# Kernel tuning notes

Measured on AMD Instinct MI355X. Metric: run time of the kernel, lower is better.

The kernel has to match this reference:

```python
import jax, jax.numpy as jnp
import numpy as np

N = 20000   # nodes
E = 400000  # edges per hop
IN_C = 256
HID = 128
HEADS = 2
OUT_C = 256
RELU_SLOPE = 0.2  # GATConv LeakyReLU negative slope
EPS = 1e-16


def _segment_mean(vals, idx, num_segments):
    s = jax.ops.segment_sum(vals, idx, num_segments=num_segments)
    cnt = jax.ops.segment_sum(jnp.ones((vals.shape[0], 1), vals.dtype), idx,
                              num_segments=num_segments)
    return s / (cnt + EPS)


def _gat(x, src, dst, Wg, a_src, a_dst, bg):
    # x: [N, IN_C] -> h: [N, HEADS, HID]
    h = (x @ Wg).reshape(N, HEADS, HID)
    alpha_s = jnp.sum(h * a_src, axis=-1)  # [N, HEADS]
    alpha_d = jnp.sum(h * a_dst, axis=-1)  # [N, HEADS]
    logits = jax.nn.leaky_relu(alpha_s[src] + alpha_d[dst], RELU_SLOPE)  # [E, HEADS]
    # softmax over incoming edges per destination node
    m = jax.ops.segment_max(logits, dst, num_segments=N)  # [N, HEADS]
    m = jnp.where(jnp.isfinite(m), m, 0.0)
    ex = jnp.exp(logits - m[dst])
    denom = jax.ops.segment_sum(ex, dst, num_segments=N)  # [N, HEADS]
    alpha = ex / (denom[dst] + EPS)  # [E, HEADS]
    msg = h[src] * alpha[..., None]  # [E, HEADS, HID]
    out = jax.ops.segment_sum(msg, dst, num_segments=N)  # [N, HEADS, HID]
    return out.reshape(N, HEADS * HID) + bg


def setup_inputs() -> dict:
    key = jax.random.key(0)
    ks = jax.random.split(key, 16)

    def xav(k, shape):
        fan_in, fan_out = shape[0], shape[-1]
        lim = np.sqrt(6.0 / (fan_in + fan_out)).astype(np.float32)
        return jax.random.uniform(k, shape, jnp.float32, -lim, lim)

    inp = {
        "x": jax.random.normal(ks[0], (N, IN_C), jnp.float32),
        "edge_index_1hop": jax.random.randint(ks[1], (2, E), 0, N),
        "edge_time_1hop": jax.random.uniform(ks[2], (E,), jnp.float32),
        "edge_index_2hop": jax.random.randint(ks[3], (2, E), 0, N),
        "edge_time_2hop": jax.random.uniform(ks[4], (E,), jnp.float32),
        "rel_embeddings": jax.random.normal(ks[5], (N, HID), jnp.float32),
        # GATConv params
        "Wg": xav(ks[6], (IN_C, HEADS * HID)),
        "a_src": jax.random.normal(ks[7], (HEADS, HID), jnp.float32) * 0.1,
        "a_dst": jax.random.normal(ks[8], (HEADS, HID), jnp.float32) * 0.1,
        "bg": jnp.zeros((HEADS * HID,), jnp.float32),
        # linear_transform
        "W_lin": xav(ks[9], (HEADS * HID, OUT_C)),
        "b_lin": jnp.zeros((OUT_C,), jnp.float32),
        # time_gate: in = 2*(OUT_C+1)
        "W_tg": xav(ks[10], (2 * (OUT_C + 1), 1)),
        "b_tg": jnp.zeros((1,), jnp.float32),
        # semantic_gate: in = (OUT_C+1) + HID + 1
        "W_sg": xav(ks[11], (OUT_C + 1 + HID + 1, 1)),
        "b_sg": jnp.zeros((1,), jnp.float32),
    }
    return inp


def reference(x, edge_index_1hop, edge_time_1hop, edge_index_2hop,
              edge_time_2hop, rel_embeddings, Wg, a_src, a_dst, bg,
              W_lin, b_lin, W_tg, b_tg, W_sg, b_sg):
    src1, dst1 = edge_index_1hop[0], edge_index_1hop[1]
    src2, dst2 = edge_index_2hop[0], edge_index_2hop[1]

    # ---- 1-hop aggregation ----
    x_1hop = _gat(x, src1, dst1, Wg, a_src, a_dst, bg) @ W_lin + b_lin  # [N, OUT_C]
    time_e1 = edge_time_1hop[:, None]  # [E, 1]
    node_time = _segment_mean(time_e1, dst1, N)  # [N, 1]
    x_1hop_t = jnp.concatenate([x_1hop, node_time], axis=-1)  # [N, OUT_C+1]

    # ---- semantic gate (per 1-hop edge -> per node) ----
    combined = jnp.concatenate(
        [x_1hop_t[src1], rel_embeddings[dst1], time_e1], axis=-1)  # [E, OUT_C+1+HID+1]
    sem_w_edge = jax.nn.sigmoid(combined @ W_sg + b_sg)  # [E, 1]
    sem_w_node = _segment_mean(sem_w_edge, dst1, N)  # [N, 1]

    # ---- 2-hop aggregation, semantically weighted ----
    x_2hop = _gat(x, src2, dst2, Wg, a_src, a_dst, bg) @ W_lin + b_lin  # [N, OUT_C]
    x_2hop = x_2hop * sem_w_node
    x_2hop_t = jnp.concatenate([x_2hop, node_time], axis=-1)  # [N, OUT_C+1]

    # ---- time-gated fusion ----
    gate_in = jnp.concatenate([x_1hop_t, x_2hop_t], axis=-1)  # [N, 2*(OUT_C+1)]
    g = jax.nn.sigmoid(gate_in @ W_tg + b_tg)  # [N, 1]
    return g * x_2hop_t + (1.0 - g) * x_1hop_t
```

## Files before the change

### kernel.cpp

```cpp
#include <hip/hip_runtime.h>
#include <math.h>

constexpr float EPSF = 1e-16f;
#define MAXDEG 64
#define BINCH 4096
#define NBUCK 64

typedef __attribute__((ext_vector_type(8))) short bfrag;
typedef __attribute__((ext_vector_type(4))) float ffrag;
typedef __attribute__((ext_vector_type(8))) unsigned short ushortv8;

__device__ __forceinline__ float leaky(float v){ return v >= 0.f ? v : 0.2f*v; }

__device__ __forceinline__ ushort f2bf(float f){
  union { float f; unsigned u; } v; v.f = f;
  unsigned r = (v.u + 0x7FFFu + ((v.u >> 16) & 1u)) >> 16;
  return (ushort)r;
}
__device__ __forceinline__ float bf2f(ushort u){
  union { unsigned u; float f; } v; v.u = ((unsigned)u) << 16;
  return v.f;
}

__device__ __forceinline__ float wred_max(float v){
  #pragma unroll
  for (int d = 32; d; d >>= 1) v = fmaxf(v, __shfl_xor(v, d));
  return v;
}
__device__ __forceinline__ float wred_sum(float v){
  #pragma unroll
  for (int d = 32; d; d >>= 1) v += __shfl_xor(v, d);
  return v;
}


__global__ __launch_bounds__(256) void k_prep(const float* __restrict__ Wg, const float* __restrict__ Wlin,
    const float* __restrict__ rel, const float* __restrict__ Wsg,
    ushort* __restrict__ Wgt, ushort* __restrict__ Wlt, float* __restrict__ p2,
    float4* __restrict__ zbase, int znum4, int ZB, int N){
  __shared__ float tile[32][33];
  int b = blockIdx.x, t = threadIdx.x;
  if (b < ZB){
    int idx = b*256 + t;
    if (idx < znum4) zbase[idx] = make_float4(0.f,0.f,0.f,0.f);
  } else if (b < ZB + 128){
    int bb = b - ZB;
    const float* W = (bb < 64) ? Wg : Wlin;
    ushort* Wt = (bb < 64) ? Wgt : Wlt;
    bb &= 63;
    int bx = (bb & 7)*32, by = (bb >> 3)*32;
    int tx = t & 31, ty = t >> 5;
    for (int r = ty; r < 32; r += 8) tile[r][tx] = W[(size_t)(by+r)*256 + bx+tx];
    __syncthreads();
    for (int r = ty; r < 32; r += 8) Wt[(size_t)(bx+r)*256 + by+tx] = f2bf(tile[tx][r]);
  } else {
    int node = (b-ZB-128)*4 + (t>>6);
    if (node >= N) return;
    int lane = t & 63;
    const float* rr = rel + (size_t)node*128;
    float q = rr[lane]*Wsg[257+lane] + rr[64+lane]*Wsg[321+lane];
    q = wred_sum(q);
    if (lane == 0) p2[node] = q;
  }
}


__global__ __launch_bounds__(256) void k_work1(const float* __restrict__ x, const ushort* __restrict__ Wgt,
    const float* __restrict__ a_src, const float* __restrict__ a_dst,
    ushort* __restrict__ hb, float* __restrict__ as_, float* __restrict__ ad_,
    const int* __restrict__ ei1, const float* __restrict__ et1, const int* __restrict__ ei2,
    int* __restrict__ gcur, int2* __restrict__ bkt1, int2* __restrict__ bkt2,
    int cap1, int cap2, int N, int E1, int E2, int GB1, int B1, int NB){
  __shared__ int hist[NBUCK];
  __shared__ int loff[NBUCK+1];
  __shared__ int cur[NBUCK];
  __shared__ int gbase_s[NBUCK];
  __shared__ int2 stage[BINCH];
  int bid = blockIdx.x, t = threadIdx.x;
  if (bid >= GB1){
    int hop = (bid >= GB1 + B1);
    int cb  = hop ? (bid - GB1 - B1) : (bid - GB1);
    const int* src_arr = hop ? ei2 : ei1;
    const int* dst_arr = hop ? (ei2 + E2) : (ei1 + E1);
    int Eh = hop ? E2 : E1;
    int c0 = cb * BINCH;
    int M = Eh - c0; if (M > BINCH) M = BINCH;
    if (t < NBUCK) hist[t] = 0;
    __syncthreads();
    #pragma unroll
    for (int k = 0; k < BINCH/256; k++){
      int i = k*256 + t;
      if (i < M) atomicAdd(&hist[dst_arr[c0 + i] / NB], 1);
    }
    __syncthreads();
    if (t < NBUCK){
      int v = hist[t];
      int xx = v;
      #pragma unroll
      for (int d = 1; d < NBUCK; d <<= 1){
        int y = __shfl_up(xx, d);
        if (t >= d) xx += y;
      }
      loff[t+1] = xx;
      if (t == 0) loff[0] = 0;
      cur[t] = xx - v;
      gbase_s[t] = atomicAdd(&gcur[hop*NBUCK + t], v);
    }
    __syncthreads();
    #pragma unroll
    for (int k = 0; k < BINCH/256; k++){
      int i = k*256 + t;
      if (i < M){
        int s = src_arr[c0 + i];
        int d = dst_arr[c0 + i];
        int b = d / NB;
        int ld = d - b*NB;
        int pos = atomicAdd(&cur[b], 1);
        float tv = hop ? 0.f : et1[c0 + i];
        stage[pos] = make_int2(s | (ld << 15), __float_as_int(tv));
      }
    }
    __syncthreads();
    int2* bkt = hop ? bkt2 : bkt1;
    int cap = hop ? cap2 : cap1;
    for (int s = t; s < M; s += 256){
      int lo = 0, hi = NBUCK;
      while (hi - lo > 1){ int mid = (lo + hi) >> 1; if (loff[mid] <= s) lo = mid; else hi = mid; }
      int gpos = gbase_s[lo] + (s - loff[lo]);
      if (gpos < cap) bkt[(size_t)lo*cap + gpos] = stage[s];
    }
    return;
  }
  int head = bid & 1;
  int bx = bid >> 1;
  int wid = t >> 6, lane = t & 63;
  int wr = wid >> 1, wc = wid & 1;
  int row0 = bx*128 + wr*64;
  int col0 = head*128 + wc*64;
  int l15 = lane & 15, lk = lane >> 4;
  ffrag acc[4][4];
  #pragma unroll
  for (int i = 0; i < 4; i++)
    #pragma unroll
    for (int j = 0; j < 4; j++){ ffrag z; z[0]=0.f; z[1]=0.f; z[2]=0.f; z[3]=0.f; acc[i][j] = z; }
  for (int kk = 0; kk < 256; kk += 32){
    bfrag a[4], b[4];
    #pragma unroll
    for (int i = 0; i < 4; i++){
      int r = row0 + i*16 + l15; if (r > N-1) r = N-1;
      float4 u0 = *(const float4*)(x + (size_t)r*256 + kk + lk*8);
      float4 u1 = *(const float4*)(x + (size_t)r*256 + kk + lk*8 + 4);
      bfrag tv;
      tv[0]=(short)f2bf(u0.x); tv[1]=(short)f2bf(u0.y); tv[2]=(short)f2bf(u0.z); tv[3]=(short)f2bf(u0.w);
      tv[4]=(short)f2bf(u1.x); tv[5]=(short)f2bf(u1.y); tv[6]=(short)f2bf(u1.z); tv[7]=(short)f2bf(u1.w);
      a[i] = tv;
      int c = col0 + i*16 + l15;
      b[i] = *(const bfrag*)(Wgt + (size_t)c*256 + kk + lk*8);
    }
    #pragma unroll
    for (int i = 0; i < 4; i++)
      #pragma unroll
      for (int j = 0; j < 4; j++)
        acc[i][j] = __builtin_amdgcn_mfma_f32_16x16x32_bf16(a[i], b[j], acc[i][j], 0, 0, 0);
  }
  float asv[4], adv[4];
  #pragma unroll
  for (int j = 0; j < 4; j++){
    int cc = wc*64 + j*16 + l15;
    asv[j] = a_src[head*128 + cc];
    adv[j] = a_dst[head*128 + cc];
  }
  #pragma unroll
  for (int i = 0; i < 4; i++){
    float ps[4] = {0.f,0.f,0.f,0.f}, pd[4] = {0.f,0.f,0.f,0.f};
    #pragma unroll
    for (int j = 0; j < 4; j++){
      int c = col0 + j*16 + l15;
      #pragma unroll
      for (int q = 0; q < 4; q++){
        int r = row0 + i*16 + lk*4 + q;
        float v = acc[i][j][q];
        if (r < N) hb[(size_t)r*256 + c] = f2bf(v);
        ps[q] = fmaf(v, asv[j], ps[q]);
        pd[q] = fmaf(v, adv[j], pd[q]);
      }
    }
    #pragma unroll
    for (int q = 0; q < 4; q++){
      #pragma unroll
      for (int d = 1; d < 16; d <<= 1){
        ps[q] += __shfl_xor(ps[q], d);
        pd[q] += __shfl_xor(pd[q], d);
      }
      int r = row0 + i*16 + lk*4 + q;
      if (l15 == 0 && r < N){
        atomicAdd(&as_[r*2 + head], ps[q]);
        atomicAdd(&ad_[r*2 + head], pd[q]);
      }
    }
  }
}


__global__ __launch_bounds__(256) void k_place(const int* __restrict__ gcur,
    const int2* __restrict__ bkt1, const int2* __restrict__ bkt2, int cap1, int cap2,
    int* __restrict__ ssrc1, int* __restrict__ ssrc2, float* __restrict__ stime1,
    int* __restrict__ cntg, float* __restrict__ ntime, float* __restrict__ p1,
    const float* __restrict__ Wsg, int N, int NB){
  __shared__ int   cnt_l[512];
  __shared__ float ts_l[512];
  int b = blockIdx.x & 63, hop = blockIdx.x >> 6;
  int t = threadIdx.x;
  int nbase = b * NB;
  int ncnt = N - nbase; if (ncnt > NB) ncnt = NB; if (ncnt < 0) ncnt = 0;
  for (int i = t; i < NB; i += 256){ cnt_l[i] = 0; ts_l[i] = 0.f; }
  __syncthreads();
  const int2* bkt = hop ? bkt2 : bkt1;
  int cap = hop ? cap2 : cap1;
  int len = gcur[hop*NBUCK + b]; if (len > cap) len = cap;
  int* ssrc = hop ? ssrc2 : ssrc1;
  for (int i = t; i < len; i += 256){
    int2 en = bkt[(size_t)b*cap + i];
    int src = en.x & 0x7FFF;
    int ld  = en.x >> 15;
    int slot = atomicAdd(&cnt_l[ld], 1);
    if (slot < MAXDEG){
      size_t o = (size_t)(nbase + ld)*MAXDEG + slot;
      ssrc[o] = src;
      if (hop == 0) stime1[o] = __int_as_float(en.y);
    }
    if (hop == 0) atomicAdd(&ts_l[ld], __int_as_float(en.y));
  }
  __syncthreads();
  float w256 = Wsg[256];
  for (int ld = t; ld < ncnt; ld += 256){
    int node = nbase + ld;
    int c = cnt_l[ld];
    cntg[hop*N + node] = c;
    if (hop == 0){
      float nt = ts_l[ld] / ((float)c + EPSF);
      ntime[node] = nt;
      p1[node] = nt * w256;
    }
  }
}


__global__ __launch_bounds__(256) void k_node(const int* __restrict__ cntg,
    const int* __restrict__ ssrc1, const int* __restrict__ ssrc2,
    const float* __restrict__ as_, const float* __restrict__ ad_,
    const ushort* __restrict__ h, const float* __restrict__ bg,
    ushort* __restrict__ gatb, int N, int gN4){
  __shared__ int   s_src[4][MAXDEG];
  __shared__ float2 s_w[4][MAXDEG];
  int wid = threadIdx.x >> 6, lane = threadIdx.x & 63;
  int hop = blockIdx.x >= gN4;
  int node = (blockIdx.x - (hop ? gN4 : 0))*4 + wid;
  bool active = node < N;
  const int* ssrc = hop ? ssrc2 : ssrc1;
  int deg = 0; float ad0 = 0.f, ad1 = 0.f;
  if (active){
    int degt = cntg[hop*N + node];
    deg = degt > MAXDEG ? MAXDEG : degt;
    ad0 = ad_[node*2]; ad1 = ad_[node*2+1];
  }
  size_t o0 = (size_t)node * MAXDEG;
  int msrc = 0;
  float l0 = -INFINITY, l1 = -INFINITY;
  if (lane < deg){
    msrc = ssrc[o0 + lane];
    float2 a = ((const float2*)as_)[msrc];
    l0 = leaky(a.x + ad0); l1 = leaky(a.y + ad1);
  }
  float m0 = wred_max(l0), m1 = wred_max(l1);
  float x0 = 0.f, x1 = 0.f;
  if (lane < deg){ x0 = __expf(l0 - m0); x1 = __expf(l1 - m1); }
  float e0 = wred_sum(x0), e1 = wred_sum(x1);
  float rd0 = 1.f/(e0 + EPSF), rd1 = 1.f/(e1 + EPSF);
  s_src[wid][lane] = msrc;
  s_w[wid][lane] = make_float2(x0*rd0, x1*rd1);
  if (!active) return;
  int eh = lane >> 5, cl = lane & 31, ch0 = cl << 3, head = cl >> 4;
  float acc[8] = {0.f,0.f,0.f,0.f,0.f,0.f,0.f,0.f};
  int i = 0;
  for (; i + 8 <= deg; i += 8){
    int eA = i + eh, eB = i + 2 + eh, eC = i + 4 + eh, eD = i + 6 + eh;
    int sA = s_src[wid][eA], sB = s_src[wid][eB];
    int sC = s_src[wid][eC], sD = s_src[wid][eD];
    float2 wA2 = s_w[wid][eA], wB2 = s_w[wid][eB];
    float2 wC2 = s_w[wid][eC], wD2 = s_w[wid][eD];
    float wA = head ? wA2.y : wA2.x;
    float wB = head ? wB2.y : wB2.x;
    float wC = head ? wC2.y : wC2.x;
    float wD = head ? wD2.y : wD2.x;
    ushortv8 uA = *(const ushortv8*)(h + (size_t)sA*256 + ch0);
    ushortv8 uB = *(const ushortv8*)(h + (size_t)sB*256 + ch0);
    ushortv8 uC = *(const ushortv8*)(h + (size_t)sC*256 + ch0);
    ushortv8 uD = *(const ushortv8*)(h + (size_t)sD*256 + ch0);
    #pragma unroll
    for (int k = 0; k < 8; k++) acc[k] = fmaf(wA, bf2f(uA[k]), acc[k]);
    #pragma unroll
    for (int k = 0; k < 8; k++) acc[k] = fmaf(wB, bf2f(uB[k]), acc[k]);
    #pragma unroll
    for (int k = 0; k < 8; k++) acc[k] = fmaf(wC, bf2f(uC[k]), acc[k]);
    #pragma unroll
    for (int k = 0; k < 8; k++) acc[k] = fmaf(wD, bf2f(uD[k]), acc[k]);
  }
  for (; i + 4 <= deg; i += 4){
    int eA = i + eh, eB = i + 2 + eh;
    int sA = s_src[wid][eA], sB = s_src[wid][eB];
    float2 wA2 = s_w[wid][eA], wB2 = s_w[wid][eB];
    float wA = head ? wA2.y : wA2.x;
    float wB = head ? wB2.y : wB2.x;
    ushortv8 uA = *(const ushortv8*)(h + (size_t)sA*256 + ch0);
    ushortv8 uB = *(const ushortv8*)(h + (size_t)sB*256 + ch0);
    #pragma unroll
    for (int k = 0; k < 8; k++) acc[k] = fmaf(wA, bf2f(uA[k]), acc[k]);
    #pragma unroll
    for (int k = 0; k < 8; k++) acc[k] = fmaf(wB, bf2f(uB[k]), acc[k]);
  }
  for (; i < deg; i += 2){
    int e = i + eh;
    bool v = e < deg;
    int s = v ? s_src[wid][e] : 0;
    float w = 0.f;
    if (v){ float2 w2 = s_w[wid][e]; w = head ? w2.y : w2.x; }
    ushortv8 u = *(const ushortv8*)(h + (size_t)s*256 + ch0);
    #pragma unroll
    for (int k = 0; k < 8; k++) acc[k] = fmaf(w, bf2f(u[k]), acc[k]);
  }
  #pragma unroll
  for (int k = 0; k < 8; k++) acc[k] += __shfl_xor(acc[k], 32);
  if (eh == 0){
    float4 b0 = *(const float4*)(bg + ch0);
    float4 b1 = *(const float4*)(bg + ch0 + 4);
    ushortv8 o;
    o[0] = f2bf(acc[0] + b0.x); o[1] = f2bf(acc[1] + b0.y);
    o[2] = f2bf(acc[2] + b0.z); o[3] = f2bf(acc[3] + b0.w);
    o[4] = f2bf(acc[4] + b1.x); o[5] = f2bf(acc[5] + b1.y);
    o[6] = f2bf(acc[6] + b1.z); o[7] = f2bf(acc[7] + b1.w);
    *(ushortv8*)(gatb + (size_t)(hop ? N + node : node)*256 + ch0) = o;
  }
}


__global__ __launch_bounds__(256) void k_gemm2(const ushort* __restrict__ A, const ushort* __restrict__ Bt,
    const float* __restrict__ bias, const float* __restrict__ Wsg,
    ushort* __restrict__ Cb, float* __restrict__ p1, int M, int N){
  int wid = threadIdx.x >> 6, lane = threadIdx.x & 63;
  int wr = wid >> 1, wc = wid & 1;
  int row0 = blockIdx.x*128 + wr*64;
  int col0 = blockIdx.y*128 + wc*64;
  int l15 = lane & 15, lk = lane >> 4;
  ffrag acc[4][4];
  #pragma unroll
  for (int i = 0; i < 4; i++)
    #pragma unroll
    for (int j = 0; j < 4; j++){ ffrag z; z[0]=0.f; z[1]=0.f; z[2]=0.f; z[3]=0.f; acc[i][j] = z; }
  for (int kk = 0; kk < 256; kk += 32){
    bfrag a[4], b[4];
    #pragma unroll
    for (int i = 0; i < 4; i++){
      int r = row0 + i*16 + l15; if (r > M-1) r = M-1;
      a[i] = *(const bfrag*)(A + (size_t)r*256 + kk + lk*8);
      int c = col0 + i*16 + l15;
      b[i] = *(const bfrag*)(Bt + (size_t)c*256 + kk + lk*8);
    }
    #pragma unroll
    for (int i = 0; i < 4; i++)
      #pragma unroll
      for (int j = 0; j < 4; j++)
        acc[i][j] = __builtin_amdgcn_mfma_f32_16x16x32_bf16(a[i], b[j], acc[i][j], 0, 0, 0);
  }
  float wsv[4]; float bv[4];
  #pragma unroll
  for (int j = 0; j < 4; j++){
    int c = col0 + j*16 + l15;
    wsv[j] = Wsg[c];
    bv[j] = bias[c];
  }
  #pragma unroll
  for (int i = 0; i < 4; i++){
    float ps[4] = {0.f,0.f,0.f,0.f};
    #pragma unroll
    for (int j = 0; j < 4; j++){
      int c = col0 + j*16 + l15;
      #pragma unroll
      for (int q = 0; q < 4; q++){
        int r = row0 + i*16 + lk*4 + q;
        float v = acc[i][j][q] + bv[j];
        if (r < M) Cb[(size_t)r*256 + c] = f2bf(v);
        ps[q] = fmaf(v, wsv[j], ps[q]);
      }
    }
    #pragma unroll
    for (int q = 0; q < 4; q++){
      #pragma unroll
      for (int d = 1; d < 16; d <<= 1) ps[q] += __shfl_xor(ps[q], d);
      int r = row0 + i*16 + lk*4 + q;
      if (l15 == 0 && r < N) atomicAdd(&p1[r], ps[q]);
    }
  }
}


__global__ __launch_bounds__(256) void k_final(const ushort* __restrict__ x1, const ushort* __restrict__ x2r,
    const int* __restrict__ cntg, const int* __restrict__ ssrc1, const float* __restrict__ stime1,
    const float* __restrict__ p1, const float* __restrict__ p2,
    const float* __restrict__ Wsg, const float* __restrict__ bsg,
    const float* __restrict__ ntime, const float* __restrict__ Wtg, const float* __restrict__ btg,
    float* __restrict__ out, int N){
  int node = blockIdx.x*4 + (threadIdx.x>>6);
  if (node >= N) return;
  int lane = threadIdx.x & 63;
  int degt = cntg[node];
  int deg = degt > MAXDEG ? MAXDEG : degt;
  float acc = 0.f;
  if (lane < deg){
    size_t o = (size_t)node*MAXDEG + lane;
    float z = p1[ssrc1[o]] + p2[node] + bsg[0] + stime1[o]*Wsg[385];
    acc = 1.f / (1.f + __expf(-z));
  }
  acc = wred_sum(acc);
  float sm = acc / ((float)degt + EPSF);
  float nt = ntime[node];
  int c0 = lane << 2;
  ushort4 au = *(const ushort4*)(x1  + (size_t)node*256 + c0);
  ushort4 ru = *(const ushort4*)(x2r + (size_t)node*256 + c0);
  float4 a4 = make_float4(bf2f(au.x), bf2f(au.y), bf2f(au.z), bf2f(au.w));
  float4 b4; b4.x = bf2f(ru.x)*sm; b4.y = bf2f(ru.y)*sm; b4.z = bf2f(ru.z)*sm; b4.w = bf2f(ru.w)*sm;
  float4 w1 = *(const float4*)(Wtg + c0);
  float4 w2 = *(const float4*)(Wtg + 257 + c0);
  float s = a4.x*w1.x + a4.y*w1.y + a4.z*w1.z + a4.w*w1.w
          + b4.x*w2.x + b4.y*w2.y + b4.z*w2.z + b4.w*w2.w;
  if (lane == 0) s += nt*Wtg[256] + nt*Wtg[513] + btg[0];
  s = wred_sum(s);
  float g = 1.f / (1.f + __expf(-s));
  float* orow = out + (size_t)node*257;
  orow[c0+0] = g*b4.x + (1.f - g)*a4.x;
  orow[c0+1] = g*b4.y + (1.f - g)*a4.y;
  orow[c0+2] = g*b4.z + (1.f - g)*a4.z;
  orow[c0+3] = g*b4.w + (1.f - g)*a4.w;
  if (lane == 0) orow[256] = nt;
}


extern "C" void kernel_launch(void* const* d_in, const int* in_sizes, int n_in,
                              void* d_out, int out_size, void* d_ws, size_t ws_size,
                              hipStream_t stream){
  const float* x    = (const float*)d_in[0];
  const int*   ei1  = (const int*)d_in[1];
  const float* et1  = (const float*)d_in[2];
  const int*   ei2  = (const int*)d_in[3];
  const float* rel  = (const float*)d_in[5];
  const float* Wg   = (const float*)d_in[6];
  const float* asrc = (const float*)d_in[7];
  const float* adst = (const float*)d_in[8];
  const float* bg   = (const float*)d_in[9];
  const float* Wlin = (const float*)d_in[10];
  const float* blin = (const float*)d_in[11];
  const float* Wtg  = (const float*)d_in[12];
  const float* btg  = (const float*)d_in[13];
  const float* Wsg  = (const float*)d_in[14];
  const float* bsg  = (const float*)d_in[15];
  float* out = (float*)d_out;

  const int N  = in_sizes[0] / 256;
  const int E1 = in_sizes[1] / 2;
  const int E2 = in_sizes[3] / 2;
  const int NB = (N + NBUCK - 1) / NBUCK;
  const int cap1 = E1/NBUCK + 2048;
  const int cap2 = E2/NBUCK + 2048;

  char* base = (char*)d_ws;
  size_t off = 0;
  auto alloc = [&](size_t bytes)->char*{
    char* p = base + off;
    off += (bytes + 255) & ~(size_t)255;
    return p;
  };
  int*    gcur  = (int*)alloc((size_t)2*NBUCK*4);
  float*  as_   = (float*)alloc((size_t)2*N*4);
  float*  ad_   = (float*)alloc((size_t)2*N*4);
  size_t zero_bytes = off;
  ushort* Wgt   = (ushort*)alloc((size_t)256*256*2);
  ushort* Wlt   = (ushort*)alloc((size_t)256*256*2);
  ushort* hb    = (ushort*)alloc((size_t)N*256*2);
  ushort* gatb  = (ushort*)alloc((size_t)2*N*256*2);
  ushort* x12   = (ushort*)alloc((size_t)2*N*256*2);
  float*  ntime = (float*)alloc((size_t)N*4);
  float*  p1    = (float*)alloc((size_t)N*4);
  float*  p2    = (float*)alloc((size_t)N*4);
  int*    cntg  = (int*)alloc((size_t)2*N*4);
  int*    ssrc1 = (int*)alloc((size_t)N*MAXDEG*4);
  int*    ssrc2 = (int*)alloc((size_t)N*MAXDEG*4);
  float*  stime1= (float*)alloc((size_t)N*MAXDEG*4);
  int2*   bkt1  = (int2*)alloc((size_t)NBUCK*cap1*8);
  int2*   bkt2  = (int2*)alloc((size_t)NBUCK*cap2*8);

  dim3 blk(256);
  int gN4 = (N + 3) / 4;
  int GB1 = ((N + 127) / 128) * 2;
  int B1  = (E1 + BINCH - 1) / BINCH;
  int B2  = (E2 + BINCH - 1) / BINCH;
  int znum4 = (int)(zero_bytes / 16);
  int ZB = (znum4 + 255) / 256;
  dim3 ggemm2((2*N + 127) / 128, 2);

  k_prep<<<ZB + 128 + gN4, blk, 0, stream>>>(Wg, Wlin, rel, Wsg, Wgt, Wlt, p2,
                                             (float4*)d_ws, znum4, ZB, N);
  k_work1<<<GB1 + B1 + B2, blk, 0, stream>>>(x, Wgt, asrc, adst, hb, as_, ad_,
                                             ei1, et1, ei2, gcur, bkt1, bkt2,
                                             cap1, cap2, N, E1, E2, GB1, B1, NB);
  k_place<<<128, blk, 0, stream>>>(gcur, bkt1, bkt2, cap1, cap2, ssrc1, ssrc2, stime1,
                                   cntg, ntime, p1, Wsg, N, NB);
  k_node<<<2*gN4, blk, 0, stream>>>(cntg, ssrc1, ssrc2, as_, ad_, hb, bg, gatb, N, gN4);
  k_gemm2<<<ggemm2, blk, 0, stream>>>(gatb, Wlt, blin, Wsg, x12, p1, 2*N, N);
  k_final<<<gN4, blk, 0, stream>>>(x12, x12 + (size_t)N*256, cntg, ssrc1, stime1,
                                   p1, p2, Wsg, bsg, ntime, Wtg, btg, out, N);
}
```

Before: 149.4 us.

## Fold W_lin·W_sg into a precomputed vector and compute p1 in node kernel

Precomputes wv = W_lin·Wsg[0:256] and the bias constant in k_prep, so the semantic-gate term p1 is computed in k_node from the fp32 GAT output rather than by atomics in the GEMM epilogue. This removes the per-row shuffle reductions and atomicAdds from k_gemm2. It also rewrites the k_node gather accumulation into packed float2 multiply-adds with bit-shift bf16 unpacking and a per-head weight layout, and drops the 4-edge tail loop. The reassociation slightly changes rounding, since p1 now uses fp32 values before the bf16 GEMM.

```diff
diff --git a/kernel.cpp b/kernel.cpp
--- a/kernel.cpp
+++ b/kernel.cpp
@@ -8,6 +8,7 @@
 
 typedef __attribute__((ext_vector_type(8))) short bfrag;
 typedef __attribute__((ext_vector_type(4))) float ffrag;
+typedef __attribute__((ext_vector_type(2))) float f32x2;
 typedef __attribute__((ext_vector_type(8))) unsigned short ushortv8;
 
 __device__ __forceinline__ float leaky(float v){ return v >= 0.f ? v : 0.2f*v; }
@@ -21,6 +22,9 @@
   union { unsigned u; float f; } v; v.u = ((unsigned)u) << 16;
   return v.f;
 }
+__device__ __forceinline__ float asf(unsigned u){
+  union { unsigned u; float f; } v; v.u = u; return v.f;
+}
 
 __device__ __forceinline__ float wred_max(float v){
   #pragma unroll
@@ -35,8 +39,9 @@
 
 
 __global__ __launch_bounds__(256) void k_prep(const float* __restrict__ Wg, const float* __restrict__ Wlin,
-    const float* __restrict__ rel, const float* __restrict__ Wsg,
+    const float* __restrict__ blin, const float* __restrict__ rel, const float* __restrict__ Wsg,
     ushort* __restrict__ Wgt, ushort* __restrict__ Wlt, float* __restrict__ p2,
+    float* __restrict__ wv, float* __restrict__ wvc,
     float4* __restrict__ zbase, int znum4, int ZB, int N){
   __shared__ float tile[32][33];
   int b = blockIdx.x, t = threadIdx.x;
@@ -53,8 +58,27 @@
     for (int r = ty; r < 32; r += 8) tile[r][tx] = W[(size_t)(by+r)*256 + bx+tx];
     __syncthreads();
     for (int r = ty; r < 32; r += 8) Wt[(size_t)(bx+r)*256 + by+tx] = f2bf(tile[tx][r]);
+  } else if (b == ZB + 128){
+    __shared__ float sWsg[256];
+    __shared__ float wsum[4];
+    sWsg[t] = Wsg[t];
+    __syncthreads();
+    float acc = 0.f;
+    const float* row = Wlin + (size_t)t*256;
+    for (int c = 0; c < 256; c += 4){
+      acc = fmaf(row[c],   sWsg[c],   acc);
+      acc = fmaf(row[c+1], sWsg[c+1], acc);
+      acc = fmaf(row[c+2], sWsg[c+2], acc);
+      acc = fmaf(row[c+3], sWsg[c+3], acc);
+    }
+    wv[t] = acc;
+    float pc = blin[t]*sWsg[t];
+    pc = wred_sum(pc);
+    if ((t & 63) == 0) wsum[t >> 6] = pc;
+    __syncthreads();
+    if (t == 0) wvc[0] = wsum[0] + wsum[1] + wsum[2] + wsum[3];
   } else {
-    int node = (b-ZB-128)*4 + (t>>6);
+    int node = (b-ZB-129)*4 + (t>>6);
     if (node >= N) return;
     int lane = t & 63;
     const float* rr = rel + (size_t)node*128;
@@ -205,8 +229,7 @@
 __global__ __launch_bounds__(256) void k_place(const int* __restrict__ gcur,
     const int2* __restrict__ bkt1, const int2* __restrict__ bkt2, int cap1, int cap2,
     int* __restrict__ ssrc1, int* __restrict__ ssrc2, float* __restrict__ stime1,
-    int* __restrict__ cntg, float* __restrict__ ntime, float* __restrict__ p1,
-    const float* __restrict__ Wsg, int N, int NB){
+    int* __restrict__ cntg, float* __restrict__ ntime, int N, int NB){
   __shared__ int   cnt_l[512];
   __shared__ float ts_l[512];
   int b = blockIdx.x & 63, hop = blockIdx.x >> 6;
@@ -232,16 +255,11 @@
     if (hop == 0) atomicAdd(&ts_l[ld], __int_as_float(en.y));
   }
   __syncthreads();
-  float w256 = Wsg[256];
   for (int ld = t; ld < ncnt; ld += 256){
     int node = nbase + ld;
     int c = cnt_l[ld];
     cntg[hop*N + node] = c;
-    if (hop == 0){
-      float nt = ts_l[ld] / ((float)c + EPSF);
-      ntime[node] = nt;
-      p1[node] = nt * w256;
-    }
+    if (hop == 0) ntime[node] = ts_l[ld] / ((float)c + EPSF);
   }
 }
 
@@ -250,9 +268,11 @@
     const int* __restrict__ ssrc1, const int* __restrict__ ssrc2,
     const float* __restrict__ as_, const float* __restrict__ ad_,
     const ushort* __restrict__ h, const float* __restrict__ bg,
-    ushort* __restrict__ gatb, int N, int gN4){
+    const float* __restrict__ wv, const float* __restrict__ wvc,
+    const float* __restrict__ Wsg, const float* __restrict__ ntime,
+    ushort* __restrict__ gatb, float* __restrict__ p1, int N, int gN4){
   __shared__ int   s_src[4][MAXDEG];
-  __shared__ float2 s_w[4][MAXDEG];
+  __shared__ float s_wf[4][2][MAXDEG];
   int wid = threadIdx.x >> 6, lane = threadIdx.x & 63;
   int hop = blockIdx.x >= gN4;
   int node = (blockIdx.x - (hop ? gN4 : 0))*4 + wid;
@@ -276,77 +296,99 @@
   float x0 = 0.f, x1 = 0.f;
   if (lane < deg){ x0 = __expf(l0 - m0); x1 = __expf(l1 - m1); }
   float e0 = wred_sum(x0), e1 = wred_sum(x1);
-  float rd0 = 1.f/(e0 + EPSF), rd1 = 1.f/(e1 + EPSF);
   s_src[wid][lane] = msrc;
-  s_w[wid][lane] = make_float2(x0*rd0, x1*rd1);
+  s_wf[wid][0][lane] = x0 / (e0 + EPSF);
+  s_wf[wid][1][lane] = x1 / (e1 + EPSF);
   if (!active) return;
   int eh = lane >> 5, cl = lane & 31, ch0 = cl << 3, head = cl >> 4;
-  float acc[8] = {0.f,0.f,0.f,0.f,0.f,0.f,0.f,0.f};
+  const float* wrow = s_wf[wid][head];
+  const int*   srow = s_src[wid];
+  f32x2 acc2[4];
+  #pragma unroll
+  for (int j = 0; j < 4; j++){ acc2[j][0] = 0.f; acc2[j][1] = 0.f; }
+  union UV { ushortv8 v; unsigned d[4]; };
   int i = 0;
   for (; i + 8 <= deg; i += 8){
     int eA = i + eh, eB = i + 2 + eh, eC = i + 4 + eh, eD = i + 6 + eh;
-    int sA = s_src[wid][eA], sB = s_src[wid][eB];
-    int sC = s_src[wid][eC], sD = s_src[wid][eD];
-    float2 wA2 = s_w[wid][eA], wB2 = s_w[wid][eB];
-    float2 wC2 = s_w[wid][eC], wD2 = s_w[wid][eD];
-    float wA = head ? wA2.y : wA2.x;
-    float wB = head ? wB2.y : wB2.x;
-    float wC = head ? wC2.y : wC2.x;
-    float wD = head ? wD2.y : wD2.x;
-    ushortv8 uA = *(const ushortv8*)(h + (size_t)sA*256 + ch0);
-    ushortv8 uB = *(const ushortv8*)(h + (size_t)sB*256 + ch0);
-    ushortv8 uC = *(const ushortv8*)(h + (size_t)sC*256 + ch0);
-    ushortv8 uD = *(const ushortv8*)(h + (size_t)sD*256 + ch0);
-    #pragma unroll
-    for (int k = 0; k < 8; k++) acc[k] = fmaf(wA, bf2f(uA[k]), acc[k]);
-    #pragma unroll
-    for (int k = 0; k < 8; k++) acc[k] = fmaf(wB, bf2f(uB[k]), acc[k]);
-    #pragma unroll
-    for (int k = 0; k < 8; k++) acc[k] = fmaf(wC, bf2f(uC[k]), acc[k]);
-    #pragma unroll
-    for (int k = 0; k < 8; k++) acc[k] = fmaf(wD, bf2f(uD[k]), acc[k]);
-  }
-  for (; i + 4 <= deg; i += 4){
-    int eA = i + eh, eB = i + 2 + eh;
-    int sA = s_src[wid][eA], sB = s_src[wid][eB];
-    float2 wA2 = s_w[wid][eA], wB2 = s_w[wid][eB];
-    float wA = head ? wA2.y : wA2.x;
-    float wB = head ? wB2.y : wB2.x;
-    ushortv8 uA = *(const ushortv8*)(h + (size_t)sA*256 + ch0);
-    ushortv8 uB = *(const ushortv8*)(h + (size_t)sB*256 + ch0);
-    #pragma unroll
-    for (int k = 0; k < 8; k++) acc[k] = fmaf(wA, bf2f(uA[k]), acc[k]);
-    #pragma unroll
-    for (int k = 0; k < 8; k++) acc[k] = fmaf(wB, bf2f(uB[k]), acc[k]);
+    int sA = srow[eA], sB = srow[eB], sC = srow[eC], sD = srow[eD];
+    float wA = wrow[eA], wB = wrow[eB], wC = wrow[eC], wD = wrow[eD];
+    UV uA, uB, uC, uD;
+    uA.v = *(const ushortv8*)(h + (size_t)sA*256 + ch0);
+    uB.v = *(const ushortv8*)(h + (size_t)sB*256 + ch0);
+    uC.v = *(const ushortv8*)(h + (size_t)sC*256 + ch0);
+    uD.v = *(const ushortv8*)(h + (size_t)sD*256 + ch0);
+    f32x2 wA2 = {wA,wA}, wB2 = {wB,wB}, wC2 = {wC,wC}, wD2 = {wD,wD};
+    #pragma unroll
+    for (int j = 0; j < 4; j++){
+      f32x2 hv;
+      hv[0] = asf(uA.d[j] << 16); hv[1] = asf(uA.d[j] & 0xffff0000u);
+      acc2[j] += hv * wA2;
+    }
+    #pragma unroll
+    for (int j = 0; j < 4; j++){
+      f32x2 hv;
+      hv[0] = asf(uB.d[j] << 16); hv[1] = asf(uB.d[j] & 0xffff0000u);
+      acc2[j] += hv * wB2;
+    }
+    #pragma unroll
+    for (int j = 0; j < 4; j++){
+      f32x2 hv;
+      hv[0] = asf(uC.d[j] << 16); hv[1] = asf(uC.d[j] & 0xffff0000u);
+      acc2[j] += hv * wC2;
+    }
+    #pragma unroll
+    for (int j = 0; j < 4; j++){
+      f32x2 hv;
+      hv[0] = asf(uD.d[j] << 16); hv[1] = asf(uD.d[j] & 0xffff0000u);
+      acc2[j] += hv * wD2;
+    }
   }
   for (; i < deg; i += 2){
     int e = i + eh;
     bool v = e < deg;
-    int s = v ? s_src[wid][e] : 0;
-    float w = 0.f;
-    if (v){ float2 w2 = s_w[wid][e]; w = head ? w2.y : w2.x; }
-    ushortv8 u = *(const ushortv8*)(h + (size_t)s*256 + ch0);
-    #pragma unroll
-    for (int k = 0; k < 8; k++) acc[k] = fmaf(w, bf2f(u[k]), acc[k]);
-  }
-  #pragma unroll
-  for (int k = 0; k < 8; k++) acc[k] += __shfl_xor(acc[k], 32);
+    int s = v ? srow[e] : 0;
+    float w = v ? wrow[e] : 0.f;
+    UV u; u.v = *(const ushortv8*)(h + (size_t)s*256 + ch0);
+    f32x2 w2 = {w, w};
+    #pragma unroll
+    for (int j = 0; j < 4; j++){
+      f32x2 hv;
+      hv[0] = asf(u.d[j] << 16); hv[1] = asf(u.d[j] & 0xffff0000u);
+      acc2[j] += hv * w2;
+    }
+  }
+  #pragma unroll
+  for (int j = 0; j < 4; j++){
+    acc2[j][0] += __shfl_xor(acc2[j][0], 32);
+    acc2[j][1] += __shfl_xor(acc2[j][1], 32);
+  }
   if (eh == 0){
     float4 b0 = *(const float4*)(bg + ch0);
     float4 b1 = *(const float4*)(bg + ch0 + 4);
+    float a8[8];
+    a8[0] = acc2[0][0] + b0.x; a8[1] = acc2[0][1] + b0.y;
+    a8[2] = acc2[1][0] + b0.z; a8[3] = acc2[1][1] + b0.w;
+    a8[4] = acc2[2][0] + b1.x; a8[5] = acc2[2][1] + b1.y;
+    a8[6] = acc2[3][0] + b1.z; a8[7] = acc2[3][1] + b1.w;
     ushortv8 o;
-    o[0] = f2bf(acc[0] + b0.x); o[1] = f2bf(acc[1] + b0.y);
-    o[2] = f2bf(acc[2] + b0.z); o[3] = f2bf(acc[3] + b0.w);
-    o[4] = f2bf(acc[4] + b1.x); o[5] = f2bf(acc[5] + b1.y);
-    o[6] = f2bf(acc[6] + b1.z); o[7] = f2bf(acc[7] + b1.w);
+    #pragma unroll
+    for (int k = 0; k < 8; k++) o[k] = f2bf(a8[k]);
     *(ushortv8*)(gatb + (size_t)(hop ? N + node : node)*256 + ch0) = o;
+    if (hop == 0){
+      float vs = 0.f;
+      const float* wvp = wv + ch0;
+      #pragma unroll
+      for (int k = 0; k < 8; k++) vs = fmaf(a8[k], wvp[k], vs);
+      #pragma unroll
+      for (int d = 16; d; d >>= 1) vs += __shfl_xor(vs, d);
+      if (cl == 0) p1[node] = vs + wvc[0] + ntime[node]*Wsg[256];
+    }
   }
 }
 
 
 __global__ __launch_bounds__(256) void k_gemm2(const ushort* __restrict__ A, const ushort* __restrict__ Bt,
-    const float* __restrict__ bias, const float* __restrict__ Wsg,
-    ushort* __restrict__ Cb, float* __restrict__ p1, int M, int N){
+    const float* __restrict__ bias, ushort* __restrict__ Cb, int M){
   int wid = threadIdx.x >> 6, lane = threadIdx.x & 63;
   int wr = wid >> 1, wc = wid & 1;
   int row0 = blockIdx.x*128 + wr*64;
@@ -372,33 +414,19 @@
       for (int j = 0; j < 4; j++)
         acc[i][j] = __builtin_amdgcn_mfma_f32_16x16x32_bf16(a[i], b[j], acc[i][j], 0, 0, 0);
   }
-  float wsv[4]; float bv[4];
-  #pragma unroll
-  for (int j = 0; j < 4; j++){
-    int c = col0 + j*16 + l15;
-    wsv[j] = Wsg[c];
-    bv[j] = bias[c];
-  }
+  float bv[4];
+  #pragma unroll
+  for (int j = 0; j < 4; j++) bv[j] = bias[col0 + j*16 + l15];
   #pragma unroll
   for (int i = 0; i < 4; i++){
-    float ps[4] = {0.f,0.f,0.f,0.f};
     #pragma unroll
     for (int j = 0; j < 4; j++){
       int c = col0 + j*16 + l15;
       #pragma unroll
       for (int q = 0; q < 4; q++){
         int r = row0 + i*16 + lk*4 + q;
-        float v = acc[i][j][q] + bv[j];
-        if (r < M) Cb[(size_t)r*256 + c] = f2bf(v);
-        ps[q] = fmaf(v, wsv[j], ps[q]);
+        if (r < M) Cb[(size_t)r*256 + c] = f2bf(acc[i][j][q] + bv[j]);
       }
-    }
-    #pragma unroll
-    for (int q = 0; q < 4; q++){
-      #pragma unroll
-      for (int d = 1; d < 16; d <<= 1) ps[q] += __shfl_xor(ps[q], d);
-      int r = row0 + i*16 + lk*4 + q;
-      if (l15 == 0 && r < N) atomicAdd(&p1[r], ps[q]);
     }
   }
 }
@@ -491,6 +519,8 @@
   float*  ntime = (float*)alloc((size_t)N*4);
   float*  p1    = (float*)alloc((size_t)N*4);
   float*  p2    = (float*)alloc((size_t)N*4);
+  float*  wv    = (float*)alloc((size_t)256*4);
+  float*  wvc   = (float*)alloc((size_t)4);
   int*    cntg  = (int*)alloc((size_t)2*N*4);
   int*    ssrc1 = (int*)alloc((size_t)N*MAXDEG*4);
   int*    ssrc2 = (int*)alloc((size_t)N*MAXDEG*4);
@@ -507,15 +537,16 @@
   int ZB = (znum4 + 255) / 256;
   dim3 ggemm2((2*N + 127) / 128, 2);
 
-  k_prep<<<ZB + 128 + gN4, blk, 0, stream>>>(Wg, Wlin, rel, Wsg, Wgt, Wlt, p2,
-                                             (float4*)d_ws, znum4, ZB, N);
+  k_prep<<<ZB + 129 + gN4, blk, 0, stream>>>(Wg, Wlin, blin, rel, Wsg, Wgt, Wlt, p2,
+                                             wv, wvc, (float4*)d_ws, znum4, ZB, N);
   k_work1<<<GB1 + B1 + B2, blk, 0, stream>>>(x, Wgt, asrc, adst, hb, as_, ad_,
                                              ei1, et1, ei2, gcur, bkt1, bkt2,
                                              cap1, cap2, N, E1, E2, GB1, B1, NB);
   k_place<<<128, blk, 0, stream>>>(gcur, bkt1, bkt2, cap1, cap2, ssrc1, ssrc2, stime1,
-                                   cntg, ntime, p1, Wsg, N, NB);
-  k_node<<<2*gN4, blk, 0, stream>>>(cntg, ssrc1, ssrc2, as_, ad_, hb, bg, gatb, N, gN4);
-  k_gemm2<<<ggemm2, blk, 0, stream>>>(gatb, Wlt, blin, Wsg, x12, p1, 2*N, N);
+                                   cntg, ntime, N, NB);
+  k_node<<<2*gN4, blk, 0, stream>>>(cntg, ssrc1, ssrc2, as_, ad_, hb, bg,
+                                    wv, wvc, Wsg, ntime, gatb, p1, N, gN4);
+  k_gemm2<<<ggemm2, blk, 0, stream>>>(gatb, Wlt, blin, x12, 2*N);
   k_final<<<gN4, blk, 0, stream>>>(x12, x12 + (size_t)N*256, cntg, ssrc1, stime1,
                                    p1, p2, Wsg, bsg, ntime, Wtg, btg, out, N);
 }
```

Result: slower. 155.1 us (+3.8%).

## Fuse second GEMM with final gating and precompute semantic projection via Wlin·Wsg

Applied to the files above, without the earlier changes.

Merges the second linear GEMM and the final time-gated fusion into one kernel that keeps x_1hop/x_2hop tiles in LDS, so the bf16 x12 intermediate no longer makes a round trip through global memory. The semantic-gate term p1 is now computed algebraically in k_node as the GAT output dotted with a precomputed Wlin·Wsg vector, which removes the atomics from the GEMM epilogue. In exchange the fused kernel uses a 64 KB LDS tile at 512 threads, which may lower occupancy, and the per-node gating loop runs serially within each wave.

```diff
diff --git a/kernel.cpp b/kernel.cpp
--- a/kernel.cpp
+++ b/kernel.cpp
@@ -35,10 +35,12 @@
 
 
 __global__ __launch_bounds__(256) void k_prep(const float* __restrict__ Wg, const float* __restrict__ Wlin,
-    const float* __restrict__ rel, const float* __restrict__ Wsg,
+    const float* __restrict__ blin, const float* __restrict__ rel, const float* __restrict__ Wsg,
     ushort* __restrict__ Wgt, ushort* __restrict__ Wlt, float* __restrict__ p2,
+    float* __restrict__ wv, float* __restrict__ wvc,
     float4* __restrict__ zbase, int znum4, int ZB, int N){
   __shared__ float tile[32][33];
+  __shared__ float wsum[4];
   int b = blockIdx.x, t = threadIdx.x;
   if (b < ZB){
     int idx = b*256 + t;
@@ -53,8 +55,29 @@
     for (int r = ty; r < 32; r += 8) tile[r][tx] = W[(size_t)(by+r)*256 + bx+tx];
     __syncthreads();
     for (int r = ty; r < 32; r += 8) Wt[(size_t)(bx+r)*256 + by+tx] = f2bf(tile[tx][r]);
+  } else if (b < ZB + 136){
+    int bb = b - ZB - 128;
+    int row = bb*32 + (t >> 3);
+    int c0 = (t & 7)*32;
+    const float* rp = Wlin + (size_t)row*256 + c0;
+    const float* wp = Wsg + c0;
+    float acc = 0.f;
+    #pragma unroll
+    for (int m = 0; m < 32; m += 4){
+      float4 r4 = *(const float4*)(rp + m);
+      float4 w4 = *(const float4*)(wp + m);
+      acc += r4.x*w4.x + r4.y*w4.y + r4.z*w4.z + r4.w*w4.w;
+    }
+    acc += __shfl_xor(acc, 1); acc += __shfl_xor(acc, 2); acc += __shfl_xor(acc, 4);
+    if ((t & 7) == 0) wv[row] = acc;
+  } else if (b == ZB + 136){
+    float pc = blin[t]*Wsg[t];
+    pc = wred_sum(pc);
+    if ((t & 63) == 0) wsum[t >> 6] = pc;
+    __syncthreads();
+    if (t == 0) wvc[0] = wsum[0] + wsum[1] + wsum[2] + wsum[3];
   } else {
-    int node = (b-ZB-128)*4 + (t>>6);
+    int node = (b-ZB-137)*4 + (t>>6);
     if (node >= N) return;
     int lane = t & 63;
     const float* rr = rel + (size_t)node*128;
@@ -113,9 +136,9 @@
       if (i < M){
         int s = src_arr[c0 + i];
         int d = dst_arr[c0 + i];
-        int b = d / NB;
-        int ld = d - b*NB;
-        int pos = atomicAdd(&cur[b], 1);
+        int bb = d / NB;
+        int ld = d - bb*NB;
+        int pos = atomicAdd(&cur[bb], 1);
         float tv = hop ? 0.f : et1[c0 + i];
         stage[pos] = make_int2(s | (ld << 15), __float_as_int(tv));
       }
@@ -205,8 +228,7 @@
 __global__ __launch_bounds__(256) void k_place(const int* __restrict__ gcur,
     const int2* __restrict__ bkt1, const int2* __restrict__ bkt2, int cap1, int cap2,
     int* __restrict__ ssrc1, int* __restrict__ ssrc2, float* __restrict__ stime1,
-    int* __restrict__ cntg, float* __restrict__ ntime, float* __restrict__ p1,
-    const float* __restrict__ Wsg, int N, int NB){
+    int* __restrict__ cntg, float* __restrict__ ntime, int N, int NB){
   __shared__ int   cnt_l[512];
   __shared__ float ts_l[512];
   int b = blockIdx.x & 63, hop = blockIdx.x >> 6;
@@ -232,16 +254,11 @@
     if (hop == 0) atomicAdd(&ts_l[ld], __int_as_float(en.y));
   }
   __syncthreads();
-  float w256 = Wsg[256];
   for (int ld = t; ld < ncnt; ld += 256){
     int node = nbase + ld;
     int c = cnt_l[ld];
     cntg[hop*N + node] = c;
-    if (hop == 0){
-      float nt = ts_l[ld] / ((float)c + EPSF);
-      ntime[node] = nt;
-      p1[node] = nt * w256;
-    }
+    if (hop == 0) ntime[node] = ts_l[ld] / ((float)c + EPSF);
   }
 }
 
@@ -250,8 +267,10 @@
     const int* __restrict__ ssrc1, const int* __restrict__ ssrc2,
     const float* __restrict__ as_, const float* __restrict__ ad_,
     const ushort* __restrict__ h, const float* __restrict__ bg,
-    ushort* __restrict__ gatb, int N, int gN4){
-  __shared__ int   s_src[4][MAXDEG];
+    const float* __restrict__ wv, const float* __restrict__ wvc,
+    const float* __restrict__ Wsg, const float* __restrict__ ntime,
+    ushort* __restrict__ gatb, float* __restrict__ p1, int N, int gN4){
+  __shared__ int    s_src[4][MAXDEG];
   __shared__ float2 s_w[4][MAXDEG];
   int wid = threadIdx.x >> 6, lane = threadIdx.x & 63;
   int hop = blockIdx.x >= gN4;
@@ -281,12 +300,12 @@
   s_w[wid][lane] = make_float2(x0*rd0, x1*rd1);
   if (!active) return;
   int eh = lane >> 5, cl = lane & 31, ch0 = cl << 3, head = cl >> 4;
+  const int* srow = s_src[wid];
   float acc[8] = {0.f,0.f,0.f,0.f,0.f,0.f,0.f,0.f};
   int i = 0;
   for (; i + 8 <= deg; i += 8){
     int eA = i + eh, eB = i + 2 + eh, eC = i + 4 + eh, eD = i + 6 + eh;
-    int sA = s_src[wid][eA], sB = s_src[wid][eB];
-    int sC = s_src[wid][eC], sD = s_src[wid][eD];
+    int sA = srow[eA], sB = srow[eB], sC = srow[eC], sD = srow[eD];
     float2 wA2 = s_w[wid][eA], wB2 = s_w[wid][eB];
     float2 wC2 = s_w[wid][eC], wD2 = s_w[wid][eD];
     float wA = head ? wA2.y : wA2.x;
@@ -308,7 +327,7 @@
   }
   for (; i + 4 <= deg; i += 4){
     int eA = i + eh, eB = i + 2 + eh;
-    int sA = s_src[wid][eA], sB = s_src[wid][eB];
+    int sA = srow[eA], sB = srow[eB];
     float2 wA2 = s_w[wid][eA], wB2 = s_w[wid][eB];
     float wA = head ? wA2.y : wA2.x;
     float wB = head ? wB2.y : wB2.x;
@@ -322,7 +341,7 @@
   for (; i < deg; i += 2){
     int e = i + eh;
     bool v = e < deg;
-    int s = v ? s_src[wid][e] : 0;
+    int s = v ? srow[e] : 0;
     float w = 0.f;
     if (v){ float2 w2 = s_w[wid][e]; w = head ? w2.y : w2.x; }
     ushortv8 u = *(const ushortv8*)(h + (size_t)s*256 + ch0);
@@ -334,114 +353,114 @@
   if (eh == 0){
     float4 b0 = *(const float4*)(bg + ch0);
     float4 b1 = *(const float4*)(bg + ch0 + 4);
+    float a8[8];
+    a8[0] = acc[0] + b0.x; a8[1] = acc[1] + b0.y;
+    a8[2] = acc[2] + b0.z; a8[3] = acc[3] + b0.w;
+    a8[4] = acc[4] + b1.x; a8[5] = acc[5] + b1.y;
+    a8[6] = acc[6] + b1.z; a8[7] = acc[7] + b1.w;
     ushortv8 o;
-    o[0] = f2bf(acc[0] + b0.x); o[1] = f2bf(acc[1] + b0.y);
-    o[2] = f2bf(acc[2] + b0.z); o[3] = f2bf(acc[3] + b0.w);
-    o[4] = f2bf(acc[4] + b1.x); o[5] = f2bf(acc[5] + b1.y);
-    o[6] = f2bf(acc[6] + b1.z); o[7] = f2bf(acc[7] + b1.w);
+    #pragma unroll
+    for (int k = 0; k < 8; k++) o[k] = f2bf(a8[k]);
     *(ushortv8*)(gatb + (size_t)(hop ? N + node : node)*256 + ch0) = o;
-  }
-}
-
-
-__global__ __launch_bounds__(256) void k_gemm2(const ushort* __restrict__ A, const ushort* __restrict__ Bt,
-    const float* __restrict__ bias, const float* __restrict__ Wsg,
-    ushort* __restrict__ Cb, float* __restrict__ p1, int M, int N){
-  int wid = threadIdx.x >> 6, lane = threadIdx.x & 63;
-  int wr = wid >> 1, wc = wid & 1;
-  int row0 = blockIdx.x*128 + wr*64;
-  int col0 = blockIdx.y*128 + wc*64;
-  int l15 = lane & 15, lk = lane >> 4;
-  ffrag acc[4][4];
-  #pragma unroll
-  for (int i = 0; i < 4; i++)
-    #pragma unroll
-    for (int j = 0; j < 4; j++){ ffrag z; z[0]=0.f; z[1]=0.f; z[2]=0.f; z[3]=0.f; acc[i][j] = z; }
-  for (int kk = 0; kk < 256; kk += 32){
-    bfrag a[4], b[4];
-    #pragma unroll
-    for (int i = 0; i < 4; i++){
-      int r = row0 + i*16 + l15; if (r > M-1) r = M-1;
-      a[i] = *(const bfrag*)(A + (size_t)r*256 + kk + lk*8);
-      int c = col0 + i*16 + l15;
-      b[i] = *(const bfrag*)(Bt + (size_t)c*256 + kk + lk*8);
-    }
-    #pragma unroll
-    for (int i = 0; i < 4; i++)
-      #pragma unroll
-      for (int j = 0; j < 4; j++)
-        acc[i][j] = __builtin_amdgcn_mfma_f32_16x16x32_bf16(a[i], b[j], acc[i][j], 0, 0, 0);
-  }
-  float wsv[4]; float bv[4];
-  #pragma unroll
-  for (int j = 0; j < 4; j++){
-    int c = col0 + j*16 + l15;
-    wsv[j] = Wsg[c];
-    bv[j] = bias[c];
-  }
-  #pragma unroll
-  for (int i = 0; i < 4; i++){
-    float ps[4] = {0.f,0.f,0.f,0.f};
-    #pragma unroll
-    for (int j = 0; j < 4; j++){
-      int c = col0 + j*16 + l15;
-      #pragma unroll
-      for (int q = 0; q < 4; q++){
-        int r = row0 + i*16 + lk*4 + q;
-        float v = acc[i][j][q] + bv[j];
-        if (r < M) Cb[(size_t)r*256 + c] = f2bf(v);
-        ps[q] = fmaf(v, wsv[j], ps[q]);
-      }
-    }
-    #pragma unroll
-    for (int q = 0; q < 4; q++){
-      #pragma unroll
-      for (int d = 1; d < 16; d <<= 1) ps[q] += __shfl_xor(ps[q], d);
-      int r = row0 + i*16 + lk*4 + q;
-      if (l15 == 0 && r < N) atomicAdd(&p1[r], ps[q]);
-    }
-  }
-}
-
-
-__global__ __launch_bounds__(256) void k_final(const ushort* __restrict__ x1, const ushort* __restrict__ x2r,
+    if (hop == 0){
+      float vs = 0.f;
+      const float* wvp = wv + ch0;
+      #pragma unroll
+      for (int k = 0; k < 8; k++) vs = fmaf(a8[k], wvp[k], vs);
+      #pragma unroll
+      for (int d = 16; d; d >>= 1) vs += __shfl_xor(vs, d);
+      if (cl == 0) p1[node] = vs + wvc[0] + ntime[node]*Wsg[256];
+    }
+  }
+}
+
+
+__global__ __launch_bounds__(512) void k_fused(const ushort* __restrict__ A, const ushort* __restrict__ Bt,
+    const float* __restrict__ bias,
     const int* __restrict__ cntg, const int* __restrict__ ssrc1, const float* __restrict__ stime1,
     const float* __restrict__ p1, const float* __restrict__ p2,
     const float* __restrict__ Wsg, const float* __restrict__ bsg,
     const float* __restrict__ ntime, const float* __restrict__ Wtg, const float* __restrict__ btg,
     float* __restrict__ out, int N){
-  int node = blockIdx.x*4 + (threadIdx.x>>6);
-  if (node >= N) return;
-  int lane = threadIdx.x & 63;
-  int degt = cntg[node];
-  int deg = degt > MAXDEG ? MAXDEG : degt;
-  float acc = 0.f;
-  if (lane < deg){
-    size_t o = (size_t)node*MAXDEG + lane;
-    float z = p1[ssrc1[o]] + p2[node] + bsg[0] + stime1[o]*Wsg[385];
-    acc = 1.f / (1.f + __expf(-z));
-  }
-  acc = wred_sum(acc);
-  float sm = acc / ((float)degt + EPSF);
-  float nt = ntime[node];
+  __shared__ ushort sx[2][64][256];
+  int t = threadIdx.x;
+  int w = t >> 6, lane = t & 63;
+  int wr = w >> 2, wc = w & 3;
+  int n0 = blockIdx.x*64;
+  int l15 = lane & 15, lk = lane >> 4;
+  int col0 = wc*64;
+  size_t abase = wr ? (size_t)N*256 : 0;
+  ffrag acc[4][4];
+  #pragma unroll
+  for (int i = 0; i < 4; i++)
+    #pragma unroll
+    for (int j = 0; j < 4; j++){ ffrag z; z[0]=0.f; z[1]=0.f; z[2]=0.f; z[3]=0.f; acc[i][j] = z; }
+  for (int kk = 0; kk < 256; kk += 32){
+    bfrag a[4], b[4];
+    #pragma unroll
+    for (int i = 0; i < 4; i++){
+      int gr = n0 + i*16 + l15; if (gr > N-1) gr = N-1;
+      a[i] = *(const bfrag*)(A + abase + (size_t)gr*256 + kk + lk*8);
+      int c = col0 + i*16 + l15;
+      b[i] = *(const bfrag*)(Bt + (size_t)c*256 + kk + lk*8);
+    }
+    #pragma unroll
+    for (int i = 0; i < 4; i++)
+      #pragma unroll
+      for (int j = 0; j < 4; j++)
+        acc[i][j] = __builtin_amdgcn_mfma_f32_16x16x32_bf16(a[i], b[j], acc[i][j], 0, 0, 0);
+  }
+  float bv[4];
+  #pragma unroll
+  for (int j = 0; j < 4; j++) bv[j] = bias[col0 + j*16 + l15];
+  #pragma unroll
+  for (int i = 0; i < 4; i++){
+    #pragma unroll
+    for (int j = 0; j < 4; j++){
+      int c = col0 + j*16 + l15;
+      #pragma unroll
+      for (int q = 0; q < 4; q++){
+        int lr = i*16 + lk*4 + q;
+        sx[wr][lr][c] = f2bf(acc[i][j][q] + bv[j]);
+      }
+    }
+  }
+  __syncthreads();
+  float wt385 = Wsg[385], bsg0 = bsg[0];
   int c0 = lane << 2;
-  ushort4 au = *(const ushort4*)(x1  + (size_t)node*256 + c0);
-  ushort4 ru = *(const ushort4*)(x2r + (size_t)node*256 + c0);
-  float4 a4 = make_float4(bf2f(au.x), bf2f(au.y), bf2f(au.z), bf2f(au.w));
-  float4 b4; b4.x = bf2f(ru.x)*sm; b4.y = bf2f(ru.y)*sm; b4.z = bf2f(ru.z)*sm; b4.w = bf2f(ru.w)*sm;
   float4 w1 = *(const float4*)(Wtg + c0);
   float4 w2 = *(const float4*)(Wtg + 257 + c0);
-  float s = a4.x*w1.x + a4.y*w1.y + a4.z*w1.z + a4.w*w1.w
-          + b4.x*w2.x + b4.y*w2.y + b4.z*w2.z + b4.w*w2.w;
-  if (lane == 0) s += nt*Wtg[256] + nt*Wtg[513] + btg[0];
-  s = wred_sum(s);
-  float g = 1.f / (1.f + __expf(-s));
-  float* orow = out + (size_t)node*257;
-  orow[c0+0] = g*b4.x + (1.f - g)*a4.x;
-  orow[c0+1] = g*b4.y + (1.f - g)*a4.y;
-  orow[c0+2] = g*b4.z + (1.f - g)*a4.z;
-  orow[c0+3] = g*b4.w + (1.f - g)*a4.w;
-  if (lane == 0) orow[256] = nt;
+  for (int k = 0; k < 8; k++){
+    int ln = w*8 + k;
+    int node = n0 + ln;
+    if (node >= N) break;
+    int degt = cntg[node];
+    int deg = degt > MAXDEG ? MAXDEG : degt;
+    float accs = 0.f;
+    if (lane < deg){
+      size_t o = (size_t)node*MAXDEG + lane;
+      float z = p1[ssrc1[o]] + p2[node] + bsg0 + stime1[o]*wt385;
+      accs = 1.f / (1.f + __expf(-z));
+    }
+    accs = wred_sum(accs);
+    float sm = accs / ((float)degt + EPSF);
+    float nt = ntime[node];
+    ushort4 au = *(const ushort4*)&sx[0][ln][c0];
+    ushort4 ru = *(const ushort4*)&sx[1][ln][c0];
+    float4 a4 = make_float4(bf2f(au.x), bf2f(au.y), bf2f(au.z), bf2f(au.w));
+    float4 b4; b4.x = bf2f(ru.x)*sm; b4.y = bf2f(ru.y)*sm; b4.z = bf2f(ru.z)*sm; b4.w = bf2f(ru.w)*sm;
+    float s = a4.x*w1.x + a4.y*w1.y + a4.z*w1.z + a4.w*w1.w
+            + b4.x*w2.x + b4.y*w2.y + b4.z*w2.z + b4.w*w2.w;
+    if (lane == 0) s += nt*Wtg[256] + nt*Wtg[513] + btg[0];
+    s = wred_sum(s);
+    float g = 1.f / (1.f + __expf(-s));
+    float* orow = out + (size_t)node*257;
+    orow[c0+0] = g*b4.x + (1.f - g)*a4.x;
+    orow[c0+1] = g*b4.y + (1.f - g)*a4.y;
+    orow[c0+2] = g*b4.z + (1.f - g)*a4.z;
+    orow[c0+3] = g*b4.w + (1.f - g)*a4.w;
+    if (lane == 0) orow[256] = nt;
+  }
 }
 
 
@@ -487,10 +506,11 @@
   ushort* Wlt   = (ushort*)alloc((size_t)256*256*2);
   ushort* hb    = (ushort*)alloc((size_t)N*256*2);
   ushort* gatb  = (ushort*)alloc((size_t)2*N*256*2);
-  ushort* x12   = (ushort*)alloc((size_t)2*N*256*2);
   float*  ntime = (float*)alloc((size_t)N*4);
   float*  p1    = (float*)alloc((size_t)N*4);
   float*  p2    = (float*)alloc((size_t)N*4);
+  float*  wv    = (float*)alloc((size_t)256*4);
+  float*  wvc   = (float*)alloc((size_t)4);
   int*    cntg  = (int*)alloc((size_t)2*N*4);
   int*    ssrc1 = (int*)alloc((size_t)N*MAXDEG*4);
   int*    ssrc2 = (int*)alloc((size_t)N*MAXDEG*4);
@@ -505,17 +525,17 @@
   int B2  = (E2 + BINCH - 1) / BINCH;
   int znum4 = (int)(zero_bytes / 16);
   int ZB = (znum4 + 255) / 256;
-  dim3 ggemm2((2*N + 127) / 128, 2);
-
-  k_prep<<<ZB + 128 + gN4, blk, 0, stream>>>(Wg, Wlin, rel, Wsg, Wgt, Wlt, p2,
-                                             (float4*)d_ws, znum4, ZB, N);
+  int gF = (N + 63) / 64;
+
+  k_prep<<<ZB + 137 + gN4, blk, 0, stream>>>(Wg, Wlin, blin, rel, Wsg, Wgt, Wlt, p2,
+                                             wv, wvc, (float4*)d_ws, znum4, ZB, N);
   k_work1<<<GB1 + B1 + B2, blk, 0, stream>>>(x, Wgt, asrc, adst, hb, as_, ad_,
                                              ei1, et1, ei2, gcur, bkt1, bkt2,
                                              cap1, cap2, N, E1, E2, GB1, B1, NB);
   k_place<<<128, blk, 0, stream>>>(gcur, bkt1, bkt2, cap1, cap2, ssrc1, ssrc2, stime1,
-                                   cntg, ntime, p1, Wsg, N, NB);
-  k_node<<<2*gN4, blk, 0, stream>>>(cntg, ssrc1, ssrc2, as_, ad_, hb, bg, gatb, N, gN4);
-  k_gemm2<<<ggemm2, blk, 0, stream>>>(gatb, Wlt, blin, Wsg, x12, p1, 2*N, N);
-  k_final<<<gN4, blk, 0, stream>>>(x12, x12 + (size_t)N*256, cntg, ssrc1, stime1,
-                                   p1, p2, Wsg, bsg, ntime, Wtg, btg, out, N);
-}
+                                   cntg, ntime, N, NB);
+  k_node<<<2*gN4, blk, 0, stream>>>(cntg, ssrc1, ssrc2, as_, ad_, hb, bg,
+                                    wv, wvc, Wsg, ntime, gatb, p1, N, gN4);
+  k_fused<<<gF, dim3(512), 0, stream>>>(gatb, Wlt, blin, cntg, ssrc1, stime1,
+                                        p1, p2, Wsg, bsg, ntime, Wtg, btg, out, N);
+}
```

New measurement: 158.8 us. +6.3%, slower.
